# Kernel tuning notes

Hardware: AMD Instinct MI355X
Metric: run time of the kernel (lower is better)

## Reference

```python
import jax, jax.numpy as jnp
import numpy as np
import math

N_FREQ = 50
ENC_DIM = 4 * N_FREQ  # 200
D = 5
N_GENES = 1000
N_CELLS = 5000
N_FRAG = 200_000


def sine_encoding(coords):
    # frequencies: [f1,f1,f2,f2,...] length 2*N_FREQ; shifts: [0, pi/2, 0, pi/2, ...]
    i = jnp.arange(1, N_FREQ + 1, dtype=jnp.float32)
    freqs = jnp.repeat(1.0 / jnp.power(jnp.float32(1000.0), 2.0 * i / N_FREQ), 2)
    shifts = jnp.tile(jnp.array([0.0, math.pi / 2], jnp.float32), N_FREQ)
    # coords [F,2] -> [F,2,2*nf] -> [F,4*nf]
    return jnp.sin((coords[..., None] * freqs + shifts).reshape(coords.shape[0], -1))


def self_attention(x):
    # x: [G, i, D]; NOTE: scale uses sqrt(seq_len) = sqrt(x.shape[-2]) as in the original
    scores = jnp.einsum('gid,gjd->gij', x, x) / jnp.sqrt(jnp.float32(x.shape[1]))
    w = jax.nn.softmax(scores, axis=-1)
    return jnp.einsum('gij,gjd->gid', w, x)


def setup_inputs() -> dict:
    key = jax.random.key(0)
    ks = jax.random.split(key, 6)
    coordinates = jax.random.uniform(ks[0], (N_FRAG, 2), jnp.float32, -1000.0, 1000.0)
    genemapping = jax.random.randint(ks[1], (N_FRAG,), 0, N_GENES)
    local_cellxgene_ix = jax.random.randint(ks[2], (N_FRAG,), 0, N_CELLS * N_GENES)
    genes_oi = jnp.arange(N_GENES)
    # ragged groups: disjoint fragment index sets for group sizes 2, 3, 4
    n2 = jnp.arange(60000)             # 30000 pairs
    n3 = jnp.arange(60000) + 60000     # 20000 triples
    n4 = jnp.arange(60000) + 120000    # 15000 quads
    stdv = 1.0 / math.sqrt(D)
    weight1_frag = jax.random.uniform(ks[3], (N_GENES, ENC_DIM, D), jnp.float32, -stdv, stdv)
    weight1_expr = jnp.ones((N_GENES, D), jnp.float32)
    bias1 = jax.random.normal(ks[4], (N_GENES,), jnp.float32)  # mean_gene_expression
    return dict(coordinates=coordinates, genemapping=genemapping, n2=n2, n3=n3, n4=n4,
                local_cellxgene_ix=local_cellxgene_ix, genes_oi=genes_oi,
                weight1_frag=weight1_frag, weight1_expr=weight1_expr, bias1=bias1)


def reference(coordinates, genemapping, n2, n3, n4, local_cellxgene_ix, genes_oi,
              weight1_frag, weight1_expr, bias1):
    # FragmentEmbedder: sine encode, per-gene weight gather, contract, sigmoid
    enc = sine_encoding(coordinates)                                 # [F, 200]
    emb = jax.nn.sigmoid(jnp.einsum('fe,fed->fd', enc, weight1_frag[genemapping]))  # [F, 5]
    # ragged self-attention over fixed-size groups (2, 3, 4)
    for idx, i in ((n2, 2), (n3, 3), (n4, 4)):
        x = emb[idx].reshape(-1, i, D)
        emb = emb.at[idx].set(self_attention(x).reshape(-1, D))
    # EmbeddingGenePooler: segment sum over cell x gene
    pooled = jax.ops.segment_sum(emb, local_cellxgene_ix, num_segments=N_CELLS * N_GENES)
    cell_gene_embedding = pooled.reshape(N_CELLS, N_GENES, D)
    # EmbeddingToExpression: gene-wise weighted sum + mean expression bias
    return (cell_gene_embedding * weight1_expr[genes_oi]).sum(-1) + bias1[genes_oi]
```

## Files before the change

### kernel.cpp

```cpp
#include <hip/hip_runtime.h>
#include <math.h>

#define DD 5
#define NFREQ 50
#define NB 128

__global__ __launch_bounds__(256) void blockhist_kernel(
    const int* __restrict__ gm, int F, int chunk,
    int* __restrict__ bc, int n_genes, int* __restrict__ done) {
  __shared__ int cnt[1000];
  if (blockIdx.x == 0 && threadIdx.x == 0) *done = 0;
  for (int j = threadIdx.x; j < n_genes; j += blockDim.x) cnt[j] = 0;
  __syncthreads();
  int b = blockIdx.x;
  int lo = b * chunk;
  int hi = min(F, lo + chunk);
  for (int i = lo + threadIdx.x; i < hi; i += blockDim.x)
    atomicAdd(&cnt[gm[i]], 1);
  __syncthreads();
  for (int j = threadIdx.x; j < n_genes; j += blockDim.x)
    bc[j * NB + b] = cnt[j];
}

__global__ __launch_bounds__(256) void binscan_starts_kernel(
    int* __restrict__ bc, int n_genes, int* __restrict__ totals,
    int* __restrict__ starts, int* __restrict__ done, int nblocks) {
  __shared__ int s_amlast;
  __shared__ int s_ws[4];
  int lane = threadIdx.x & 63;
  int wv = threadIdx.x >> 6;
  int bin = blockIdx.x * 4 + wv;
  if (bin < n_genes) {
    int2* row = (int2*)(bc + (size_t)bin * NB);
    int2 v = row[lane];
    int p = v.x + v.y;
    int ip = p;
#pragma unroll
    for (int off = 1; off < 64; off <<= 1) {
      int q = __shfl_up(ip, off);
      if (lane >= off) ip += q;
    }
    int base = ip - p;
    int2 e;
    e.x = base;
    e.y = base + v.x;
    row[lane] = e;
    if (lane == 63) totals[bin] = ip;
  }
  __syncthreads();
  if (threadIdx.x == 0) {
    __threadfence();
    int tk = atomicAdd(done, 1);
    s_amlast = (tk == nblocks - 1);
  }
  __syncthreads();
  if (!s_amlast) return;
  __threadfence();
  int t = threadIdx.x;
  int4 v = make_int4(0, 0, 0, 0);
  if (4 * t < n_genes) v = ((const int4*)totals)[t];
  int p = v.x + v.y + v.z + v.w;
  int ip = p;
#pragma unroll
  for (int off = 1; off < 64; off <<= 1) {
    int q = __shfl_up(ip, off);
    if (lane >= off) ip += q;
  }
  if (lane == 63) s_ws[wv] = ip;
  __syncthreads();
  int add = 0;
#pragma unroll
  for (int i = 0; i < 4; ++i)
    if (i < wv) add += s_ws[i];
  int excl = add + ip - p;
  int4 e;
  e.x = excl;
  e.y = excl + v.x;
  e.z = e.y + v.y;
  e.w = e.z + v.z;
  if (4 * t < n_genes) ((int4*)starts)[t] = e;
  if (4 * t + 4 == n_genes) starts[n_genes] = e.w + v.w;
}

__global__ __launch_bounds__(256) void blockscatter_kernel(
    const int* __restrict__ gm, const float2* __restrict__ coords,
    int F, int chunk,
    const int* __restrict__ bc, const int* __restrict__ starts,
    int* __restrict__ rank, float2* __restrict__ coords_sorted, int n_genes) {
  __shared__ int cur[1000];
  int b = blockIdx.x;
  for (int j = threadIdx.x; j < n_genes; j += blockDim.x)
    cur[j] = starts[j] + bc[j * NB + b];
  __syncthreads();
  int lo = b * chunk;
  int hi = min(F, lo + chunk);
  for (int i = lo + threadIdx.x; i < hi; i += blockDim.x) {
    int g = gm[i];
    int p = atomicAdd(&cur[g], 1);
    rank[i] = p;
    coords_sorted[p] = coords[i];
  }
}

__global__ __launch_bounds__(256) void embed_init_kernel(
    const float2* __restrict__ coords_sorted,
    const int* __restrict__ starts, const float* __restrict__ W,
    float* __restrict__ emb_sorted,
    float* __restrict__ out, const float* __restrict__ bias,
    const int* __restrict__ genes_oi, int n_genes, int total4) {
  __shared__ float s_freq[NFREQ];
  if (threadIdx.x < NFREQ)
    s_freq[threadIdx.x] = exp2f(-0.39863137f * (float)(threadIdx.x + 1));

  {
    int gtid = blockIdx.x * blockDim.x + threadIdx.x;
    int gs = gridDim.x * blockDim.x;
    for (int v4 = gtid; v4 < total4; v4 += gs) {
      int j = (v4 * 4) % n_genes;
      float4 vv;
      vv.x = bias[genes_oi[j + 0]];
      vv.y = bias[genes_oi[j + 1]];
      vv.z = bias[genes_oi[j + 2]];
      vv.w = bias[genes_oi[j + 3]];
      reinterpret_cast<float4*>(out)[v4] = vv;
    }
  }
  __syncthreads();

  int g = blockIdx.x;
  int s0 = starts[g];
  int s1 = starts[g + 1];
  const float* __restrict__ Wg = W + (size_t)g * (4 * NFREQ * DD);

  for (int i = s0 + threadIdx.x; i < s1; i += blockDim.x) {
    float2 xy = coords_sorted[i];
    float a0 = 0.f, a1 = 0.f, a2 = 0.f, a3 = 0.f, a4 = 0.f;
#pragma unroll 5
    for (int k = 0; k < NFREQ; ++k) {
      float fr = s_freq[k];
      float ax = xy.x * fr;
      float ay = xy.y * fr;
      float sx = __sinf(ax), cx = __cosf(ax);
      float sy = __sinf(ay), cy = __cosf(ay);
      const float* w0s = Wg + (2 * k) * DD;
      const float* w0c = w0s + DD;
      const float* w1s = Wg + (2 * NFREQ + 2 * k) * DD;
      const float* w1c = w1s + DD;
      a0 += sx * w0s[0] + cx * w0c[0] + sy * w1s[0] + cy * w1c[0];
      a1 += sx * w0s[1] + cx * w0c[1] + sy * w1s[1] + cy * w1c[1];
      a2 += sx * w0s[2] + cx * w0c[2] + sy * w1s[2] + cy * w1c[2];
      a3 += sx * w0s[3] + cx * w0c[3] + sy * w1s[3] + cy * w1c[3];
      a4 += sx * w0s[4] + cx * w0c[4] + sy * w1s[4] + cy * w1c[4];
    }
    float* e = emb_sorted + (size_t)i * DD;
    e[0] = 1.f / (1.f + __expf(-a0));
    e[1] = 1.f / (1.f + __expf(-a1));
    e[2] = 1.f / (1.f + __expf(-a2));
    e[3] = 1.f / (1.f + __expf(-a3));
    e[4] = 1.f / (1.f + __expf(-a4));
  }
}

template <int SZ>
__device__ __forceinline__ void attn_pool_group(
    const int* __restrict__ idx, const int* __restrict__ rank,
    const float* __restrict__ embs, const int* __restrict__ lci,
    const int* __restrict__ genes_oi, const float* __restrict__ wexpr,
    int n_genes, float* __restrict__ out) {
  int fid[SZ];
  float x[SZ][DD];
#pragma unroll
  for (int a = 0; a < SZ; ++a) {
    fid[a] = idx[a];
    const float* p = embs + (size_t)rank[fid[a]] * DD;
#pragma unroll
    for (int d = 0; d < DD; ++d) x[a][d] = p[d];
  }
  const float scale = rsqrtf((float)SZ);
#pragma unroll
  for (int a = 0; a < SZ; ++a) {
    float sc[SZ];
    float m = -1e30f;
#pragma unroll
    for (int b = 0; b < SZ; ++b) {
      float dt = 0.f;
#pragma unroll
      for (int d = 0; d < DD; ++d) dt += x[a][d] * x[b][d];
      sc[b] = dt * scale;
      m = fmaxf(m, sc[b]);
    }
    float sum = 0.f;
#pragma unroll
    for (int b = 0; b < SZ; ++b) {
      sc[b] = __expf(sc[b] - m);
      sum += sc[b];
    }
    float inv = 1.f / sum;
    float o[DD];
#pragma unroll
    for (int d = 0; d < DD; ++d) {
      float acc = 0.f;
#pragma unroll
      for (int b = 0; b < SZ; ++b) acc += sc[b] * x[b][d];
      o[d] = acc * inv;
    }
    int ix = lci[fid[a]];
    int g = genes_oi[ix % n_genes];
    const float* w = wexpr + (size_t)g * DD;
    float s = o[0] * w[0] + o[1] * w[1] + o[2] * w[2] + o[3] * w[3] + o[4] * w[4];
    atomicAdd(out + ix, s);
  }
}

__global__ __launch_bounds__(256) void attn_pool_kernel(
    const int* __restrict__ n2, int g2,
    const int* __restrict__ n3, int g3,
    const int* __restrict__ n4, int g4,
    const int* __restrict__ rank, const float* __restrict__ embs,
    const int* __restrict__ lci, const int* __restrict__ genes_oi,
    const float* __restrict__ wexpr, int n_genes,
    int gtot_frag, int F, float* __restrict__ out) {
  int gtid = blockIdx.x * blockDim.x + threadIdx.x;
  int gs = gridDim.x * blockDim.x;
  int gtot = g2 + g3 + g4;
  for (int w = gtid; w < gtot; w += gs) {
    if (w < g2)
      attn_pool_group<2>(n2 + (size_t)w * 2, rank, embs, lci, genes_oi,
                         wexpr, n_genes, out);
    else if (w < g2 + g3)
      attn_pool_group<3>(n3 + (size_t)(w - g2) * 3, rank, embs, lci, genes_oi,
                         wexpr, n_genes, out);
    else
      attn_pool_group<4>(n4 + (size_t)(w - g2 - g3) * 4, rank, embs, lci,
                         genes_oi, wexpr, n_genes, out);
  }
  for (int f = gtot_frag + gtid; f < F; f += gs) {
    const float* e = embs + (size_t)rank[f] * DD;
    int ix = lci[f];
    int g = genes_oi[ix % n_genes];
    const float* w = wexpr + (size_t)g * DD;
    float s = e[0] * w[0] + e[1] * w[1] + e[2] * w[2] + e[3] * w[3] + e[4] * w[4];
    atomicAdd(out + ix, s);
  }
}

extern "C" void kernel_launch(void* const* d_in, const int* in_sizes, int n_in,
                              void* d_out, int out_size, void* d_ws, size_t ws_size,
                              hipStream_t stream) {
  const float2* coords  = (const float2*)d_in[0];
  const int* gm         = (const int*)d_in[1];
  const int* n2         = (const int*)d_in[2];
  const int* n3         = (const int*)d_in[3];
  const int* n4         = (const int*)d_in[4];
  const int* lci        = (const int*)d_in[5];
  const int* genes_oi   = (const int*)d_in[6];
  const float* W        = (const float*)d_in[7];
  const float* wexpr    = (const float*)d_in[8];
  const float* bias     = (const float*)d_in[9];
  float* out            = (float*)d_out;

  const int F       = in_sizes[1];
  const int n_genes = in_sizes[6];
  const int g2 = in_sizes[2] / 2;
  const int g3 = in_sizes[3] / 3;
  const int g4 = in_sizes[4] / 4;
  const int gtot_frag = in_sizes[2] + in_sizes[3] + in_sizes[4];

  char* ws = (char*)d_ws;
  size_t off = 0;
  float* embs    = (float*)(ws + off);  off += (size_t)F * DD * sizeof(float);
  int* rank      = (int*)(ws + off);    off += (size_t)F * sizeof(int);
  float2* csort  = (float2*)(ws + off); off += (size_t)F * sizeof(float2);
  int* bc        = (int*)(ws + off);    off += (size_t)n_genes * NB * sizeof(int);
  off = (off + 15) & ~(size_t)15;
  int* starts    = (int*)(ws + off);    off += (size_t)(n_genes + 4) * sizeof(int);
  off = (off + 15) & ~(size_t)15;
  int* totals    = (int*)(ws + off);    off += (size_t)n_genes * sizeof(int);
  int* done      = (int*)(ws + off);    off += 4 * sizeof(int);

  const int tb = 256;
  const int chunk = (F + NB - 1) / NB;
  int total4 = out_size / 4;

  blockhist_kernel<<<NB, tb, 0, stream>>>(gm, F, chunk, bc, n_genes, done);
  int scan_blocks = (n_genes + 3) / 4;
  binscan_starts_kernel<<<scan_blocks, tb, 0, stream>>>(bc, n_genes, totals,
                                                        starts, done, scan_blocks);
  blockscatter_kernel<<<NB, tb, 0, stream>>>(gm, coords, F, chunk, bc, starts,
                                             rank, csort, n_genes);
  embed_init_kernel<<<n_genes, tb, 0, stream>>>(csort, starts, W, embs,
                                                out, bias, genes_oi,
                                                n_genes, total4);
  attn_pool_kernel<<<1024, tb, 0, stream>>>(n2, g2, n3, g3, n4, g4,
                                            rank, embs, lci, genes_oi, wexpr,
                                            n_genes, gtot_frag, F, out);
}
```

Before: 144.8 us.

## Merge bin scan and scatter into one kernel with grid-wide barrier

Replaces the separate per-gene scan kernel and scatter kernel with one 128-block kernel. Each block scans a share of the per-gene histogram rows, waits at a software grid barrier built from atomics, then redundantly computes the global gene start offsets in shared memory before scattering. This removes one kernel launch and the global round-trip for the starts array. It relies on all 128 blocks being resident at the same time so the spin barrier cannot deadlock, and it repeats the totals scan in every block.

```diff
diff --git a/kernel.cpp b/kernel.cpp
--- a/kernel.cpp
+++ b/kernel.cpp
@@ -7,9 +7,9 @@
 
 __global__ __launch_bounds__(256) void blockhist_kernel(
     const int* __restrict__ gm, int F, int chunk,
-    int* __restrict__ bc, int n_genes, int* __restrict__ done) {
+    int* __restrict__ bc, int n_genes, int* __restrict__ bar) {
   __shared__ int cnt[1000];
-  if (blockIdx.x == 0 && threadIdx.x == 0) *done = 0;
+  if (blockIdx.x == 0 && threadIdx.x == 0) { bar[0] = 0; bar[1] = 0; }
   for (int j = threadIdx.x; j < n_genes; j += blockDim.x) cnt[j] = 0;
   __syncthreads();
   int b = blockIdx.x;
@@ -22,81 +22,96 @@
     bc[j * NB + b] = cnt[j];
 }
 
-__global__ __launch_bounds__(256) void binscan_starts_kernel(
-    int* __restrict__ bc, int n_genes, int* __restrict__ totals,
-    int* __restrict__ starts, int* __restrict__ done, int nblocks) {
-  __shared__ int s_amlast;
+__global__ __launch_bounds__(256) void scanscatter_kernel(
+    const int* __restrict__ gm, const float2* __restrict__ coords,
+    int F, int chunk, int* __restrict__ bc, int* __restrict__ totals,
+    int* __restrict__ starts, int* __restrict__ rank,
+    float2* __restrict__ coords_sorted, int n_genes, int* __restrict__ bar) {
+  __shared__ int s_cur[1000];
+  __shared__ int s_starts[1001];
   __shared__ int s_ws[4];
-  int lane = threadIdx.x & 63;
-  int wv = threadIdx.x >> 6;
-  int bin = blockIdx.x * 4 + wv;
-  if (bin < n_genes) {
-    int2* row = (int2*)(bc + (size_t)bin * NB);
-    int2 v = row[lane];
-    int p = v.x + v.y;
+  const int b = blockIdx.x;
+  const int lane = threadIdx.x & 63;
+  const int wv = threadIdx.x >> 6;
+
+#pragma unroll
+  for (int r = 0; r < 2; ++r) {
+    int bin = b * 4 + wv + r * 512;
+    if (bin < n_genes) {
+      int2* row = (int2*)(bc + (size_t)bin * NB);
+      int2 v = row[lane];
+      int p = v.x + v.y;
+      int ip = p;
+#pragma unroll
+      for (int off = 1; off < 64; off <<= 1) {
+        int q = __shfl_up(ip, off);
+        if (lane >= off) ip += q;
+      }
+      int base = ip - p;
+      int2 e;
+      e.x = base;
+      e.y = base + v.x;
+      row[lane] = e;
+      if (lane == 63) totals[bin] = ip;
+    }
+  }
+
+  __syncthreads();
+  if (threadIdx.x == 0) {
+    __threadfence();
+    if (atomicAdd(&bar[0], 1) == (int)gridDim.x - 1)
+      atomicExch(&bar[1], 1);
+    while (atomicAdd(&bar[1], 0) == 0)
+      __builtin_amdgcn_s_sleep(2);
+    __threadfence();
+  }
+  __syncthreads();
+
+  {
+    int t = threadIdx.x;
+    int4 v = make_int4(0, 0, 0, 0);
+    if (4 * t < n_genes) v = ((const int4*)totals)[t];
+    int p = v.x + v.y + v.z + v.w;
     int ip = p;
 #pragma unroll
     for (int off = 1; off < 64; off <<= 1) {
       int q = __shfl_up(ip, off);
       if (lane >= off) ip += q;
     }
-    int base = ip - p;
-    int2 e;
-    e.x = base;
-    e.y = base + v.x;
-    row[lane] = e;
-    if (lane == 63) totals[bin] = ip;
-  }
-  __syncthreads();
-  if (threadIdx.x == 0) {
-    __threadfence();
-    int tk = atomicAdd(done, 1);
-    s_amlast = (tk == nblocks - 1);
-  }
-  __syncthreads();
-  if (!s_amlast) return;
-  __threadfence();
-  int t = threadIdx.x;
-  int4 v = make_int4(0, 0, 0, 0);
-  if (4 * t < n_genes) v = ((const int4*)totals)[t];
-  int p = v.x + v.y + v.z + v.w;
-  int ip = p;
-#pragma unroll
-  for (int off = 1; off < 64; off <<= 1) {
-    int q = __shfl_up(ip, off);
-    if (lane >= off) ip += q;
-  }
-  if (lane == 63) s_ws[wv] = ip;
-  __syncthreads();
-  int add = 0;
-#pragma unroll
-  for (int i = 0; i < 4; ++i)
-    if (i < wv) add += s_ws[i];
-  int excl = add + ip - p;
-  int4 e;
-  e.x = excl;
-  e.y = excl + v.x;
-  e.z = e.y + v.y;
-  e.w = e.z + v.z;
-  if (4 * t < n_genes) ((int4*)starts)[t] = e;
-  if (4 * t + 4 == n_genes) starts[n_genes] = e.w + v.w;
-}
-
-__global__ __launch_bounds__(256) void blockscatter_kernel(
-    const int* __restrict__ gm, const float2* __restrict__ coords,
-    int F, int chunk,
-    const int* __restrict__ bc, const int* __restrict__ starts,
-    int* __restrict__ rank, float2* __restrict__ coords_sorted, int n_genes) {
-  __shared__ int cur[1000];
-  int b = blockIdx.x;
+    if (lane == 63) s_ws[wv] = ip;
+    __syncthreads();
+    int add = 0;
+#pragma unroll
+    for (int i = 0; i < 4; ++i)
+      if (i < wv) add += s_ws[i];
+    int excl = add + ip - p;
+    int4 e;
+    e.x = excl;
+    e.y = excl + v.x;
+    e.z = e.y + v.y;
+    e.w = e.z + v.z;
+    if (4 * t < n_genes) {
+      s_starts[4 * t + 0] = e.x;
+      s_starts[4 * t + 1] = e.y;
+      s_starts[4 * t + 2] = e.z;
+      s_starts[4 * t + 3] = e.w;
+      if (b == 0) ((int4*)starts)[t] = e;
+    }
+    if (4 * t + 4 == n_genes) {
+      s_starts[n_genes] = e.w + v.w;
+      if (b == 0) starts[n_genes] = e.w + v.w;
+    }
+  }
+  __syncthreads();
+
   for (int j = threadIdx.x; j < n_genes; j += blockDim.x)
-    cur[j] = starts[j] + bc[j * NB + b];
+    s_cur[j] = s_starts[j] + bc[(size_t)j * NB + b];
   __syncthreads();
   int lo = b * chunk;
   int hi = min(F, lo + chunk);
   for (int i = lo + threadIdx.x; i < hi; i += blockDim.x) {
     int g = gm[i];
-    int p = atomicAdd(&cur[g], 1);
+    int p = atomicAdd(&s_cur[g], 1);
     rank[i] = p;
     coords_sorted[p] = coords[i];
   }
@@ -276,18 +291,15 @@
   int* starts    = (int*)(ws + off);    off += (size_t)(n_genes + 4) * sizeof(int);
   off = (off + 15) & ~(size_t)15;
   int* totals    = (int*)(ws + off);    off += (size_t)n_genes * sizeof(int);
-  int* done      = (int*)(ws + off);    off += 4 * sizeof(int);
+  int* bar       = (int*)(ws + off);    off += 4 * sizeof(int);
 
   const int tb = 256;
   const int chunk = (F + NB - 1) / NB;
   int total4 = out_size / 4;
 
-  blockhist_kernel<<<NB, tb, 0, stream>>>(gm, F, chunk, bc, n_genes, done);
-  int scan_blocks = (n_genes + 3) / 4;
-  binscan_starts_kernel<<<scan_blocks, tb, 0, stream>>>(bc, n_genes, totals,
-                                                        starts, done, scan_blocks);
-  blockscatter_kernel<<<NB, tb, 0, stream>>>(gm, coords, F, chunk, bc, starts,
-                                             rank, csort, n_genes);
+  blockhist_kernel<<<NB, tb, 0, stream>>>(gm, F, chunk, bc, n_genes, bar);
+  scanscatter_kernel<<<NB, tb, 0, stream>>>(gm, coords, F, chunk, bc, totals,
+                                            starts, rank, csort, n_genes, bar);
   embed_init_kernel<<<n_genes, tb, 0, stream>>>(csort, starts, W, embs,
                                                 out, bias, genes_oi,
                                                 n_genes, total4);
```

Result: no change. 143.5 us (-0.9%).
